# Kernel optimization log

Hardware: AMD Instinct MI355X
Metric: run time of the kernel (lower is better)

Reference implementation:

```python
import jax, jax.numpy as jnp
import numpy as np

N = 2048
H = W = 128


def setup_inputs() -> dict:
    key = jax.random.key(0)
    ks = jax.random.split(key, 8)
    # Gaussians placed in front of a pinhole camera at the origin (+z forward)
    xy = jax.random.normal(ks[0], (N, 2), dtype=jnp.float32) * 1.5
    z = jax.random.uniform(ks[1], (N, 1), dtype=jnp.float32, minval=2.0, maxval=6.0)
    mean = jnp.concatenate([xy, z], axis=-1)
    qvec = jax.random.normal(ks[2], (N, 4), dtype=jnp.float32)
    # raw scales -> exp activation gives scales around 0.05
    svec_raw = jax.random.normal(ks[3], (N, 3), dtype=jnp.float32) * 0.3 - 3.0
    color_raw = jax.random.normal(ks[4], (N, 3), dtype=jnp.float32)
    alpha_raw = jax.random.normal(ks[5], (N,), dtype=jnp.float32)
    bg = jax.random.uniform(ks[6], (3,), dtype=jnp.float32)
    viewmat = jnp.eye(4, dtype=jnp.float32)
    intrins = jnp.array([120.0, 120.0, W / 2.0, H / 2.0], dtype=jnp.float32)  # fx fy cx cy
    return dict(mean=mean, qvec=qvec, svec_raw=svec_raw, color_raw=color_raw,
                alpha_raw=alpha_raw, bg=bg, viewmat=viewmat, intrins=intrins)


def _quat_to_rotmat(q):
    q = q / jnp.linalg.norm(q, axis=-1, keepdims=True)
    w, x, y, z = q[..., 0], q[..., 1], q[..., 2], q[..., 3]
    R = jnp.stack([
        1 - 2 * (y * y + z * z), 2 * (x * y - w * z), 2 * (x * z + w * y),
        2 * (x * y + w * z), 1 - 2 * (x * x + z * z), 2 * (y * z - w * x),
        2 * (x * z - w * y), 2 * (y * z + w * x), 1 - 2 * (x * x + y * y),
    ], axis=-1)
    return R.reshape(q.shape[:-1] + (3, 3))


def reference(mean, qvec, svec_raw, color_raw, alpha_raw, bg, viewmat, intrins):
    fx, fy, cx, cy = intrins[0], intrins[1], intrins[2], intrins[3]
    # activations used by GaussianSplattingRenderer (svec_act=exp, alpha/color=sigmoid)
    svec = jnp.exp(svec_raw)
    alpha = jax.nn.sigmoid(alpha_raw)
    color = jax.nn.sigmoid(color_raw)

    Rw = viewmat[:3, :3]
    tw = viewmat[:3, 3]
    p_cam = mean @ Rw.T + tw                      # (N,3)
    x, y, z = p_cam[:, 0], p_cam[:, 1], p_cam[:, 2]
    zc = jnp.maximum(z, 1e-3)

    # 3D covariance Sigma = R diag(s)^2 R^T  via  M = R diag(s),  Sigma = M M^T
    Rq = _quat_to_rotmat(qvec)                    # (N,3,3)
    M = Rq * svec[:, None, :]                     # (N,3,3)

    # perspective Jacobian (EWA splatting), composed with view rotation
    zeros = jnp.zeros_like(zc)
    J = jnp.stack([
        jnp.stack([fx / zc, zeros, -fx * x / (zc * zc)], axis=-1),
        jnp.stack([zeros, fy / zc, -fy * y / (zc * zc)], axis=-1),
    ], axis=-2)                                   # (N,2,3)
    T = jnp.einsum('nij,jk->nik', J, Rw)          # (N,2,3)
    TM = jnp.einsum('nij,njk->nik', T, M)         # (N,2,3)
    cov2d = jnp.einsum('nij,nkj->nik', TM, TM)    # (N,2,2)
    cov2d = cov2d + 0.3 * jnp.eye(2, dtype=cov2d.dtype)  # low-pass filter

    a = cov2d[:, 0, 0]; b = cov2d[:, 0, 1]; c = cov2d[:, 1, 1]
    det = a * c - b * b
    det_safe = jnp.maximum(det, 1e-8)
    conic_a = c / det_safe; conic_b = -b / det_safe; conic_c = a / det_safe

    # projected 2D means
    u = fx * x / zc + cx
    v = fy * y / zc + cy

    px = jnp.arange(W, dtype=jnp.float32) + 0.5
    py = jnp.arange(H, dtype=jnp.float32) + 0.5
    dx = px[:, None] - u[None, :]                 # (W,N)
    dy = py[:, None] - v[None, :]                 # (H,N)

    power = (-0.5 * (conic_a * dx * dx)[None, :, :]
             - 0.5 * (conic_c * dy * dy)[:, None, :]
             - conic_b[None, None, :] * dx[None, :, :] * dy[:, None, :])  # (H,W,N)
    g = jnp.exp(jnp.minimum(power, 0.0))
    valid = (z > 0.2) & (det > 0)
    alpha_pix = jnp.where(valid[None, None, :], jnp.minimum(0.99, alpha * g), 0.0)

    # front-to-back depth order, sequential alpha compositing via cumprod
    order = jnp.argsort(z)
    alpha_s = alpha_pix[:, :, order]              # (H,W,N)
    color_s = color[order]                        # (N,3)
    Tcum = jnp.cumprod(1.0 - alpha_s, axis=-1)
    Tprev = jnp.concatenate([jnp.ones_like(Tcum[..., :1]), Tcum[..., :-1]], axis=-1)
    wgt = alpha_s * Tprev                         # (H,W,N)
    img = jnp.einsum('hwn,nc->hwc', wgt, color_s) + Tcum[..., -1:] * bg
    return img
```

## Files before the change

### kernel.cpp

```cpp
#include <hip/hip_runtime.h>
#include <math.h>

#define NG 2048
#define IMG_W 128
#define IMG_H 128
#define L2E 1.4426950408889634f
#define BLK 1024
#define NWAVE 16

typedef unsigned long long u64;

__device__ __forceinline__ float rlf(float x, int i) {
    return __int_as_float(__builtin_amdgcn_readlane(__float_as_int(x), i));
}

struct PrepOut {
    float u, v, A, B, C, al, cr, cg, cb, z, r2;
};

template <bool COLORS>
__device__ __forceinline__ PrepOut prep_g(
    int g,
    const float* __restrict__ mean, const float* __restrict__ qvec,
    const float* __restrict__ svec_raw, const float* __restrict__ color_raw,
    const float* __restrict__ alpha_raw,
    float fx, float fy, float cx, float cy,
    float R00, float R01, float R02, float t0,
    float R10, float R11, float R12, float t1,
    float R20, float R21, float R22, float t2)
{
    PrepOut o;
    float mx = mean[g * 3 + 0], my = mean[g * 3 + 1], mz = mean[g * 3 + 2];
    float x = R00 * mx + R01 * my + R02 * mz + t0;
    float y = R10 * mx + R11 * my + R12 * mz + t1;
    float z = R20 * mx + R21 * my + R22 * mz + t2;
    float zc = fmaxf(z, 0.001f);

    float qw = qvec[g * 4 + 0], qx = qvec[g * 4 + 1];
    float qy = qvec[g * 4 + 2], qz = qvec[g * 4 + 3];
    float qn = rsqrtf(qw * qw + qx * qx + qy * qy + qz * qz);
    qw *= qn; qx *= qn; qy *= qn; qz *= qn;
    float Rq00 = 1.f - 2.f * (qy * qy + qz * qz), Rq01 = 2.f * (qx * qy - qw * qz), Rq02 = 2.f * (qx * qz + qw * qy);
    float Rq10 = 2.f * (qx * qy + qw * qz), Rq11 = 1.f - 2.f * (qx * qx + qz * qz), Rq12 = 2.f * (qy * qz - qw * qx);
    float Rq20 = 2.f * (qx * qz - qw * qy), Rq21 = 2.f * (qy * qz + qw * qx), Rq22 = 1.f - 2.f * (qx * qx + qy * qy);

    float s0 = expf(svec_raw[g * 3 + 0]);
    float s1 = expf(svec_raw[g * 3 + 1]);
    float s2 = expf(svec_raw[g * 3 + 2]);
    float M00 = Rq00 * s0, M01 = Rq01 * s1, M02 = Rq02 * s2;
    float M10 = Rq10 * s0, M11 = Rq11 * s1, M12 = Rq12 * s2;
    float M20 = Rq20 * s0, M21 = Rq21 * s1, M22 = Rq22 * s2;

    float iz = 1.0f / zc;
    float J00 = fx * iz, J02 = -fx * x * iz * iz;
    float J11 = fy * iz, J12 = -fy * y * iz * iz;
    float T00 = J00 * R00 + J02 * R20;
    float T01 = J00 * R01 + J02 * R21;
    float T02 = J00 * R02 + J02 * R22;
    float T10 = J11 * R10 + J12 * R20;
    float T11 = J11 * R11 + J12 * R21;
    float T12 = J11 * R12 + J12 * R22;
    float TM00 = T00 * M00 + T01 * M10 + T02 * M20;
    float TM01 = T00 * M01 + T01 * M11 + T02 * M21;
    float TM02 = T00 * M02 + T01 * M12 + T02 * M22;
    float TM10 = T10 * M00 + T11 * M10 + T12 * M20;
    float TM11 = T10 * M01 + T11 * M11 + T12 * M21;
    float TM12 = T10 * M02 + T11 * M12 + T12 * M22;
    float a = TM00 * TM00 + TM01 * TM01 + TM02 * TM02 + 0.3f;
    float b = TM00 * TM10 + TM01 * TM11 + TM02 * TM12;
    float c = TM10 * TM10 + TM11 * TM11 + TM12 * TM12 + 0.3f;
    float det = a * c - b * b;
    float det_safe = fmaxf(det, 1e-8f);
    float inv_det = 1.0f / det_safe;
    bool valid = (z > 0.2f) && (det > 0.0f);

    float conic_a = c * inv_det;
    float conic_b = -b * inv_det;
    float conic_c = a * inv_det;

    float half_tr = 0.5f * (conic_a + conic_c);
    float half_df = 0.5f * (conic_a - conic_c);
    float lam_min = half_tr - sqrtf(half_df * half_df + conic_b * conic_b);
    float r2 = (lam_min > 1e-20f) ? (1.05f * 2.0f * 24.0f / (L2E * lam_min)) : 3.0e38f;
    if (!valid) r2 = -1.0f;

    o.u = fx * x * iz + cx;
    o.v = fy * y * iz + cy;
    o.A = -0.5f * L2E * conic_a;
    o.B = -L2E * conic_b;
    o.C = -0.5f * L2E * conic_c;
    o.z = z;
    o.r2 = r2;
    if (COLORS) {
        o.al = 1.0f / (1.0f + expf(-alpha_raw[g]));
        o.cr = 1.0f / (1.0f + expf(-color_raw[g * 3 + 0]));
        o.cg = 1.0f / (1.0f + expf(-color_raw[g * 3 + 1]));
        o.cb = 1.0f / (1.0f + expf(-color_raw[g * 3 + 2]));
    } else {
        o.al = o.cr = o.cg = o.cb = 0.f;
    }
    return o;
}

template <int NO>
__device__ __forceinline__ void sort_ranks(const u64* zkey,
                                           unsigned short* ssid,
                                           int K, int t)
{
    u64 myk[NO];
    int myr[NO];
#pragma unroll
    for (int o = 0; o < NO; ++o) {
        int j = t + BLK * o;
        myk[o] = (j < K) ? zkey[j] : ~0ull;
        myr[o] = 0;
    }
    const ulonglong2* z2 = (const ulonglong2*)zkey;
    const int np = (K + 1) >> 1;
    for (int i = 0; i < np; ++i) {
        ulonglong2 kk = z2[i];
#pragma unroll
        for (int o = 0; o < NO; ++o) {
            myr[o] += (kk.x < myk[o]) ? 1 : 0;
            myr[o] += (kk.y < myk[o]) ? 1 : 0;
        }
    }
#pragma unroll
    for (int o = 0; o < NO; ++o) {
        int j = t + BLK * o;
        if (j < K) ssid[myr[o]] = (unsigned short)(myk[o] & 0xFFFFu);
    }
}

__global__ __launch_bounds__(BLK) void splat_kernel(
    const float* __restrict__ mean, const float* __restrict__ qvec,
    const float* __restrict__ svec_raw, const float* __restrict__ color_raw,
    const float* __restrict__ alpha_raw, const float* __restrict__ bg,
    const float* __restrict__ viewmat, const float* __restrict__ intrins,
    float* __restrict__ out)
{
    __shared__ __align__(16) u64 zkey[NG + 2];
    __shared__ unsigned short ssid[NG];
    __shared__ float4 part[NWAVE][64];
    __shared__ int scnt;

    const int t = threadIdx.x;
    const int wave = t >> 6;
    const int lane = t & 63;
    const int tx = blockIdx.x, ty = blockIdx.y;

    if (t == 0) scnt = 0;

    const float fx = intrins[0], fy = intrins[1], cx = intrins[2], cy = intrins[3];
    const float R00 = viewmat[0], R01 = viewmat[1], R02 = viewmat[2],  t0 = viewmat[3];
    const float R10 = viewmat[4], R11 = viewmat[5], R12 = viewmat[6],  t1 = viewmat[7];
    const float R20 = viewmat[8], R21 = viewmat[9], R22 = viewmat[10], t2 = viewmat[11];

    const float x0 = tx * 8 + 0.5f, x1 = x0 + 7.0f;
    const float y0 = ty * 8 + 0.5f, y1 = y0 + 7.0f;

    __syncthreads();

#pragma unroll
    for (int k = 0; k < NG / BLK; ++k) {
        int g = k * BLK + t;
        PrepOut p = prep_g<false>(g, mean, qvec, svec_raw, color_raw,
                                  alpha_raw, fx, fy, cx, cy,
                                  R00, R01, R02, t0, R10, R11, R12, t1,
                                  R20, R21, R22, t2);
        float dxm = fmaxf(0.f, fmaxf(x0 - p.u, p.u - x1));
        float dym = fmaxf(0.f, fmaxf(y0 - p.v, p.v - y1));
        if (dxm * dxm + dym * dym <= p.r2) {
            int slot = atomicAdd(&scnt, 1);
            zkey[slot] = ((u64)__float_as_uint(p.z) << 16) | (unsigned)g;
        }
    }
    __syncthreads();
    const int K = scnt;
    if (t == 0) zkey[K] = ~0ull;
    __syncthreads();

    if (K <= BLK) sort_ranks<1>(zkey, ssid, K, t);
    else          sort_ranks<2>(zkey, ssid, K, t);
    __syncthreads();

    const float fpx = tx * 8 + (lane & 7) + 0.5f;
    const float fpy = ty * 8 + (lane >> 3) + 0.5f;
    float T = 1.f, Cr = 0.f, Cg = 0.f, Cb = 0.f;

    const int Kq = (K + NWAVE - 1) / NWAVE;
    const int s0 = wave * Kq;
    const int s1 = min(K, s0 + Kq);

    for (int base = s0; base < s1; base += 64) {
        const int j = base + lane;
        const bool inr = (j < s1);
        const int idx = inr ? (int)ssid[j] : 0;
        PrepOut p = prep_g<true>(idx, mean, qvec, svec_raw, color_raw,
                                 alpha_raw, fx, fy, cx, cy,
                                 R00, R01, R02, t0, R10, R11, R12, t1,
                                 R20, R21, R22, t2);
        u64 mask = __ballot(inr);
        while (mask) {
            const int i = (int)__builtin_ctzll(mask);
            mask &= mask - 1;
            float gu = rlf(p.u, i), gv_ = rlf(p.v, i);
            float gA = rlf(p.A, i), gB = rlf(p.B, i), gC = rlf(p.C, i);
            float al = rlf(p.al, i);
            float cr = rlf(p.cr, i), cg = rlf(p.cg, i), cb = rlf(p.cb, i);

            float dx = fpx - gu;
            float dy = fpy - gv_;
            float adx2 = gA * dx * dx;
            float bdx = gB * dx;
            float pw = fminf(fmaf(dy, fmaf(gC, dy, bdx), adx2), 0.f);
            float gv = exp2f(pw);
            float a = fminf(0.99f, al * gv);
            float w = a * T;
            Cr = fmaf(w, cr, Cr); Cg = fmaf(w, cg, Cg); Cb = fmaf(w, cb, Cb);
            T = fmaf(-a, T, T);
        }
        if (__all(T < 1e-6f)) break;
    }

    part[wave][lane] = make_float4(Cr, Cg, Cb, T);
    __syncthreads();

    if (wave == 0) {
        float4 acc = part[0][lane];
#pragma unroll
        for (int s = 1; s < NWAVE; ++s) {
            float4 p = part[s][lane];
            acc.x = fmaf(acc.w, p.x, acc.x);
            acc.y = fmaf(acc.w, p.y, acc.y);
            acc.z = fmaf(acc.w, p.z, acc.z);
            acc.w *= p.w;
        }
        const int col = tx * 8 + (lane & 7);
        const int row = ty * 8 + (lane >> 3);
        const int pix = row * IMG_W + col;
        out[pix * 3 + 0] = acc.x + acc.w * bg[0];
        out[pix * 3 + 1] = acc.y + acc.w * bg[1];
        out[pix * 3 + 2] = acc.z + acc.w * bg[2];
    }
}

extern "C" void kernel_launch(void* const* d_in, const int* in_sizes, int n_in,
                              void* d_out, int out_size, void* d_ws, size_t ws_size,
                              hipStream_t stream)
{
    const float* mean      = (const float*)d_in[0];
    const float* qvec      = (const float*)d_in[1];
    const float* svec_raw  = (const float*)d_in[2];
    const float* color_raw = (const float*)d_in[3];
    const float* alpha_raw = (const float*)d_in[4];
    const float* bg        = (const float*)d_in[5];
    const float* viewmat   = (const float*)d_in[6];
    const float* intrins   = (const float*)d_in[7];
    float* out = (float*)d_out;
    (void)d_ws; (void)ws_size;

    hipLaunchKernelGGL(splat_kernel, dim3(16, 16), dim3(BLK), 0, stream,
                       mean, qvec, svec_raw, color_raw, alpha_raw, bg,
                       viewmat, intrins, out);
}
```

Baseline: 78.67 us.

## Use hardware transcendental intrinsics, tighten culling radius, skip idle waves in sort

Replaces expf, rsqrtf, sqrtf, divisions and sigmoids with AMDGPU builtin exp2, rcp, rsq and sqrt approximations, both in per-Gaussian preprocessing and in the inner compositing loop. It lowers the culling threshold from 24 to 18 log2 units, so fewer Gaussians pass into each tile's list. Waves whose thread range lies entirely beyond K now skip the rank-sort routine. The trade-off is slightly less accurate math and a tighter cutoff that drops faint Gaussian tails, which could shift output values.

Measured after the change: 75.18 us (median of 2 runs). 4.4% less time.

```diff
diff --git a/kernel.cpp b/kernel.cpp
--- a/kernel.cpp
+++ b/kernel.cpp
@@ -5,6 +5,7 @@
 #define IMG_W 128
 #define IMG_H 128
 #define L2E 1.4426950408889634f
+#define THR 18.0f
 #define BLK 1024
 #define NWAVE 16
 
@@ -13,6 +14,13 @@
 __device__ __forceinline__ float rlf(float x, int i) {
     return __int_as_float(__builtin_amdgcn_readlane(__float_as_int(x), i));
 }
+
+__device__ __forceinline__ float fexp2(float x) { return __builtin_amdgcn_exp2f(x); }
+__device__ __forceinline__ float frcp(float x)  { return __builtin_amdgcn_rcpf(x); }
+__device__ __forceinline__ float frsq(float x)  { return __builtin_amdgcn_rsqf(x); }
+__device__ __forceinline__ float fsqr(float x)  { return __builtin_amdgcn_sqrtf(x); }
+__device__ __forceinline__ float fexp(float x)  { return fexp2(x * L2E); }
+__device__ __forceinline__ float fsig(float x)  { return frcp(1.f + fexp2(-x * L2E)); }
 
 struct PrepOut {
     float u, v, A, B, C, al, cr, cg, cb, z, r2;
@@ -38,20 +46,20 @@
 
     float qw = qvec[g * 4 + 0], qx = qvec[g * 4 + 1];
     float qy = qvec[g * 4 + 2], qz = qvec[g * 4 + 3];
-    float qn = rsqrtf(qw * qw + qx * qx + qy * qy + qz * qz);
+    float qn = frsq(qw * qw + qx * qx + qy * qy + qz * qz);
     qw *= qn; qx *= qn; qy *= qn; qz *= qn;
     float Rq00 = 1.f - 2.f * (qy * qy + qz * qz), Rq01 = 2.f * (qx * qy - qw * qz), Rq02 = 2.f * (qx * qz + qw * qy);
     float Rq10 = 2.f * (qx * qy + qw * qz), Rq11 = 1.f - 2.f * (qx * qx + qz * qz), Rq12 = 2.f * (qy * qz - qw * qx);
     float Rq20 = 2.f * (qx * qz - qw * qy), Rq21 = 2.f * (qy * qz + qw * qx), Rq22 = 1.f - 2.f * (qx * qx + qy * qy);
 
-    float s0 = expf(svec_raw[g * 3 + 0]);
-    float s1 = expf(svec_raw[g * 3 + 1]);
-    float s2 = expf(svec_raw[g * 3 + 2]);
+    float s0 = fexp(svec_raw[g * 3 + 0]);
+    float s1 = fexp(svec_raw[g * 3 + 1]);
+    float s2 = fexp(svec_raw[g * 3 + 2]);
     float M00 = Rq00 * s0, M01 = Rq01 * s1, M02 = Rq02 * s2;
     float M10 = Rq10 * s0, M11 = Rq11 * s1, M12 = Rq12 * s2;
     float M20 = Rq20 * s0, M21 = Rq21 * s1, M22 = Rq22 * s2;
 
-    float iz = 1.0f / zc;
+    float iz = frcp(zc);
     float J00 = fx * iz, J02 = -fx * x * iz * iz;
     float J11 = fy * iz, J12 = -fy * y * iz * iz;
     float T00 = J00 * R00 + J02 * R20;
@@ -71,7 +79,7 @@
     float c = TM10 * TM10 + TM11 * TM11 + TM12 * TM12 + 0.3f;
     float det = a * c - b * b;
     float det_safe = fmaxf(det, 1e-8f);
-    float inv_det = 1.0f / det_safe;
+    float inv_det = frcp(det_safe);
     bool valid = (z > 0.2f) && (det > 0.0f);
 
     float conic_a = c * inv_det;
@@ -80,8 +88,8 @@
 
     float half_tr = 0.5f * (conic_a + conic_c);
     float half_df = 0.5f * (conic_a - conic_c);
-    float lam_min = half_tr - sqrtf(half_df * half_df + conic_b * conic_b);
-    float r2 = (lam_min > 1e-20f) ? (1.05f * 2.0f * 24.0f / (L2E * lam_min)) : 3.0e38f;
+    float lam_min = half_tr - fsqr(half_df * half_df + conic_b * conic_b);
+    float r2 = (lam_min > 1e-20f) ? (1.05f * 2.0f * THR / (L2E * lam_min)) : 3.0e38f;
     if (!valid) r2 = -1.0f;
 
     o.u = fx * x * iz + cx;
@@ -92,10 +100,10 @@
     o.z = z;
     o.r2 = r2;
     if (COLORS) {
-        o.al = 1.0f / (1.0f + expf(-alpha_raw[g]));
-        o.cr = 1.0f / (1.0f + expf(-color_raw[g * 3 + 0]));
-        o.cg = 1.0f / (1.0f + expf(-color_raw[g * 3 + 1]));
-        o.cb = 1.0f / (1.0f + expf(-color_raw[g * 3 + 2]));
+        o.al = fsig(alpha_raw[g]);
+        o.cr = fsig(color_raw[g * 3 + 0]);
+        o.cg = fsig(color_raw[g * 3 + 1]);
+        o.cb = fsig(color_raw[g * 3 + 2]);
     } else {
         o.al = o.cr = o.cg = o.cb = 0.f;
     }
@@ -180,8 +188,11 @@
     if (t == 0) zkey[K] = ~0ull;
     __syncthreads();
 
-    if (K <= BLK) sort_ranks<1>(zkey, ssid, K, t);
-    else          sort_ranks<2>(zkey, ssid, K, t);
+    if (K > BLK) {
+        sort_ranks<2>(zkey, ssid, K, t);
+    } else if ((t & ~63) < K) {
+        sort_ranks<1>(zkey, ssid, K, t);
+    }
     __syncthreads();
 
     const float fpx = tx * 8 + (lane & 7) + 0.5f;
@@ -214,7 +225,7 @@
             float adx2 = gA * dx * dx;
             float bdx = gB * dx;
             float pw = fminf(fmaf(dy, fmaf(gC, dy, bdx), adx2), 0.f);
-            float gv = exp2f(pw);
+            float gv = fexp2(pw);
             float a = fminf(0.99f, al * gv);
             float w = a * T;
             Cr = fmaf(w, cr, Cr); Cg = fmaf(w, cg, Cg); Cb = fmaf(w, cb, Cb);
```
